# Performance work log

Hardware: AMD Instinct MI355X
Metric: run time of the kernel (lower is better)

## Reference

```python
import jax, jax.numpy as jnp
import numpy as np

HIDDEN = 2048
NH = 32          # num attention heads
NKV = 8          # num key/value heads
HD = HIDDEN // NH  # head_dim = 64
ROPE_BASE = 10000.0
NEG_INF = -1e9


def _rope_interleaved(t, positions):
    # t: [b, s, h, d], interleaved RoPE over full head_dim (flash-attn RotaryEmbedding(interleaved=True))
    d = t.shape[-1]
    inv_freq = 1.0 / (ROPE_BASE ** (jnp.arange(0, d, 2, dtype=jnp.float32) / d))
    ang = positions[:, None].astype(jnp.float32) * inv_freq[None, :]  # [s, d/2]
    cos = jnp.cos(ang)[None, :, None, :]
    sin = jnp.sin(ang)[None, :, None, :]
    t1 = t[..., 0::2]
    t2 = t[..., 1::2]
    out_even = t1 * cos - t2 * sin
    out_odd = t1 * sin + t2 * cos
    return jnp.stack([out_even, out_odd], axis=-1).reshape(t.shape)


def setup_inputs() -> dict:
    key = jax.random.key(0)
    k1, k2, k3 = jax.random.split(key, 3)
    B, S = 2, 2048
    x = jax.random.normal(k1, (B, S, HIDDEN), dtype=jnp.float32)
    mask = jnp.ones((B, S), dtype=jnp.int32)  # padding mask, all valid
    total_head_dim = (NH + 2 * NKV) * HD  # 3072
    scale = 1.0 / np.sqrt(HIDDEN)
    w_qkv = jax.random.normal(k2, (HIDDEN, total_head_dim), dtype=jnp.float32) * scale
    w_o = jax.random.normal(k3, (NH * HD, HIDDEN), dtype=jnp.float32) * scale
    return {"x": x, "mask": mask, "w_qkv": w_qkv, "w_o": w_o}


def reference(x, mask, w_qkv, w_o):
    B, S, _ = x.shape
    kv_size = NKV * HD
    qkv = jnp.einsum('bsh,hd->bsd', x, w_qkv)
    q = qkv[..., :HIDDEN].reshape(B, S, NH, HD)
    kv = qkv[..., HIDDEN:].reshape(B, S, 2, NKV, HD)
    pos = jnp.arange(S)  # seqlen_offset = 0 (input_pos None)
    q = _rope_interleaved(q, pos)
    k = _rope_interleaved(kv[:, :, 0], pos)
    v = kv[:, :, 1]
    # GQA: expand kv heads to NH
    groups = NH // NKV
    k = jnp.repeat(k, groups, axis=2)  # [b, s, NH, HD]
    v = jnp.repeat(v, groups, axis=2)
    scores = jnp.einsum('bqhd,bkhd->bhqk', q, k) / np.sqrt(HD)
    causal = jnp.tril(jnp.ones((S, S), dtype=bool))
    key_valid = mask[:, None, None, :] > 0  # [b,1,1,k]
    scores = jnp.where(causal[None, None] & key_valid, scores, NEG_INF)
    probs = jax.nn.softmax(scores, axis=-1)
    attn = jnp.einsum('bhqk,bkhd->bqhd', probs, v)
    # pad_input writes zeros at padded query positions
    attn = attn * (mask[:, :, None, None] > 0)
    attn = attn.reshape(B, S, NH * HD)
    return jnp.einsum('bsd,dh->bsh', attn, w_o)
```

## Files before the change

### kernel.cpp

```cpp
#include <hip/hip_runtime.h>
#include <hip/hip_bf16.h>
#include <cstdint>
#include <cstddef>

typedef __attribute__((ext_vector_type(8))) short bf16x8;
typedef __attribute__((ext_vector_type(4))) float f32x4;

static constexpr int CB  = 2;
static constexpr int CS  = 2048;
static constexpr int CH  = 2048;
static constexpr int CNH = 32;
static constexpr int CNKV = 8;
static constexpr int CHD = 64;
static constexpr int CTHD = 3072;

__device__ __forceinline__ void gload_lds16(const void* g, void* l) {
  __builtin_amdgcn_global_load_lds(
      (const __attribute__((address_space(1))) unsigned int*)g,
      (__attribute__((address_space(3))) unsigned int*)l, 16, 0, 0);
}

__device__ __forceinline__ unsigned short bfbits(float f) {
  __hip_bfloat16 h = __float2bfloat16(f);
  return *(unsigned short*)&h;
}

__device__ __forceinline__ float b2f(unsigned short s) {
  const unsigned u = (unsigned)s << 16;
  return __uint_as_float(u);
}

__global__ void conv_bf16(const float* __restrict__ in, __hip_bfloat16* __restrict__ out, int n) {
  const int i = (blockIdx.x * 256 + threadIdx.x) * 4;
  if (i >= n) return;
  const float4 v = *(const float4*)(in + i);
  out[i]     = __float2bfloat16(v.x);
  out[i + 1] = __float2bfloat16(v.y);
  out[i + 2] = __float2bfloat16(v.z);
  out[i + 3] = __float2bfloat16(v.w);
}

__global__ void trig_table(float2* __restrict__ tab) {
  const int idx = blockIdx.x * 256 + threadIdx.x;
  const int s = idx >> 5, i = idx & 31;
  const float inv = exp2f(-(float)i * (13.287712379549449f / 32.0f));
  const float ang = (float)s * inv;
  tab[idx] = make_float2(cosf(ang), sinf(ang));
}

__global__ __launch_bounds__(256) void transpose_conv(const float* __restrict__ in,
                                                      __hip_bfloat16* __restrict__ out,
                                                      int R, int Cc) {
  __shared__ float t[32][33];
  const int nbx = Cc >> 5;
  const int bx = blockIdx.x % nbx, by = blockIdx.x / nbx;
  const int c0 = bx << 5, r0 = by << 5;
  const int tx = threadIdx.x & 31, ty = threadIdx.x >> 5;
#pragma unroll
  for (int j = 0; j < 32; j += 8)
    t[ty + j][tx] = in[(size_t)(r0 + ty + j) * Cc + c0 + tx];
  __syncthreads();
#pragma unroll
  for (int j = 0; j < 32; j += 8)
    out[(size_t)(c0 + ty + j) * R + r0 + tx] = __float2bfloat16(t[tx][ty + j]);
}

template <typename OutT>
__global__ __launch_bounds__(512) void gemm_ph(const __hip_bfloat16* __restrict__ A,
                                               const __hip_bfloat16* __restrict__ Bt,
                                               OutT* __restrict__ C, int M, int N, int K) {
  __shared__ __hip_bfloat16 As[2][128 * 64];
  __shared__ __hip_bfloat16 Bs[2][256 * 64];
  const int tid = threadIdx.x;
  const int lane = tid & 63;
  const int wave = tid >> 6;
  const int nTn = N >> 8;
  const int nwg = gridDim.x;
  const int wg = (blockIdx.x & 7) * (nwg >> 3) + (blockIdx.x >> 3);
  const int tm = wg / nTn, tn = wg % nTn;
  const size_t m0 = (size_t)tm * 128, n0 = (size_t)tn * 256;
  const __hip_bfloat16* Ag = A + m0 * K;
  const __hip_bfloat16* Bg = Bt + n0 * K;
  const int wr = wave >> 2, wc = wave & 3;
  const int rsel = lane & 15, hi = lane >> 4;

  f32x4 acc[4][4];
#pragma unroll
  for (int mf = 0; mf < 4; ++mf)
#pragma unroll
    for (int nf = 0; nf < 4; ++nf) acc[mf][nf] = (f32x4){0.f, 0.f, 0.f, 0.f};

  auto stageA = [&](int u) {
    const int k0 = u << 6, buf = u & 1;
#pragma unroll
    for (int i = 0; i < 2; ++i) {
      const int c = i * 512 + tid;
      const int r = c >> 3;
      const int swz = ((c & 7) ^ (r & 7)) << 3;
      gload_lds16(Ag + (size_t)r * K + k0 + swz, &As[buf][(i * 512 + wave * 64) * 8]);
    }
  };
  auto stageB = [&](int u) {
    const int k0 = u << 6, buf = u & 1;
#pragma unroll
    for (int i = 0; i < 4; ++i) {
      const int c = i * 512 + tid;
      const int r = c >> 3;
      const int swz = ((c & 7) ^ (r & 7)) << 3;
      gload_lds16(Bg + (size_t)r * K + k0 + swz, &Bs[buf][(i * 512 + wave * 64) * 8]);
    }
  };

  bf16x8 af[4][2];
  auto readA = [&](int buf) {
#pragma unroll
    for (int mf = 0; mf < 4; ++mf) {
      const int row = wr * 64 + mf * 16 + rsel;
      const int r7 = row & 7;
      af[mf][0] = *(const bf16x8*)&As[buf][row * 64 + ((hi ^ r7) << 3)];
      af[mf][1] = *(const bf16x8*)&As[buf][row * 64 + (((4 | hi) ^ r7) << 3)];
    }
  };
  auto mm = [&](int buf, int nfb) {
    bf16x8 bfr[2][2];
#pragma unroll
    for (int nf = 0; nf < 2; ++nf) {
      const int row = wc * 64 + (nfb + nf) * 16 + rsel;
      const int r7 = row & 7;
      bfr[nf][0] = *(const bf16x8*)&Bs[buf][row * 64 + ((hi ^ r7) << 3)];
      bfr[nf][1] = *(const bf16x8*)&Bs[buf][row * 64 + (((4 | hi) ^ r7) << 3)];
    }
    __builtin_amdgcn_s_setprio(1);
#pragma unroll
    for (int mf = 0; mf < 4; ++mf)
#pragma unroll
      for (int nf = 0; nf < 2; ++nf)
#pragma unroll
        for (int kk = 0; kk < 2; ++kk)
          acc[mf][nfb + nf] =
              __builtin_amdgcn_mfma_f32_16x16x32_bf16(af[mf][kk], bfr[nf][kk], acc[mf][nfb + nf], 0, 0, 0);
    __builtin_amdgcn_s_setprio(0);
  };

  const int T = K >> 7;
  const int UMAX = 2 * T;
  stageA(0); stageB(0); stageA(1); stageB(1);

  for (int t = 0; t < T; ++t) {
    const int u0 = 2 * t, u1 = 2 * t + 1;
    asm volatile("s_waitcnt vmcnt(2)" ::: "memory");
    __builtin_amdgcn_sched_barrier(0);
    __builtin_amdgcn_s_barrier();
    __builtin_amdgcn_sched_barrier(0);
    if (t >= 1) stageB(u1);
    readA(0);
    mm(0, 0);
    __builtin_amdgcn_sched_barrier(0);
    __builtin_amdgcn_s_barrier();
    __builtin_amdgcn_sched_barrier(0);
    if (u0 + 2 < UMAX) stageA(u0 + 2);
    mm(0, 2);
    if (t == T - 1) {
      asm volatile("s_waitcnt vmcnt(0)" ::: "memory");
    } else {
      asm volatile("s_waitcnt vmcnt(2)" ::: "memory");
    }
    __builtin_amdgcn_sched_barrier(0);
    __builtin_amdgcn_s_barrier();
    __builtin_amdgcn_sched_barrier(0);
    if (u0 + 2 < UMAX) stageB(u0 + 2);
    readA(1);
    mm(1, 0);
    __builtin_amdgcn_sched_barrier(0);
    __builtin_amdgcn_s_barrier();
    __builtin_amdgcn_sched_barrier(0);
    if (u1 + 2 < UMAX) stageA(u1 + 2);
    mm(1, 2);
  }

  const int rowb = hi << 2;
#pragma unroll
  for (int mf = 0; mf < 4; ++mf)
#pragma unroll
    for (int nf = 0; nf < 4; ++nf) {
      const size_t r0 = m0 + wr * 64 + mf * 16 + rowb;
      const size_t cc = n0 + wc * 64 + nf * 16 + rsel;
#pragma unroll
      for (int j = 0; j < 4; ++j) {
        const float v = acc[mf][nf][j];
        if constexpr (sizeof(OutT) == 4)
          C[(r0 + j) * N + cc] = v;
        else
          C[(r0 + j) * N + cc] = __float2bfloat16(v);
      }
    }
}

__global__ void rope_extract(const __hip_bfloat16* __restrict__ qkv,
                             const float2* __restrict__ tab,
                             __hip_bfloat16* __restrict__ Q,
                             __hip_bfloat16* __restrict__ Kr) {
  const int idx = blockIdx.x * 256 + threadIdx.x;
  const int t8 = idx & 7;
  const int hs = (idx >> 3) % 40;
  const int r = idx / (40 * 8);
  const int srow = r & (CS - 1);
  const int b = r >> 11;
  const int colbase = (hs < CNH) ? hs * CHD : CH + (hs - CNH) * CHD;
  const bf16x8 v = *(const bf16x8*)(qkv + (size_t)r * CTHD + colbase + t8 * 8);
  const float2* tp = tab + srow * 32 + t8 * 4;
  const float scl = (hs < CNH) ? 0.18033688011112042f : 1.0f;
  union { unsigned short u[8]; bf16x8 v8; } o;
#pragma unroll
  for (int p = 0; p < 4; ++p) {
    const float t1 = b2f((unsigned short)v[2 * p]);
    const float t2 = b2f((unsigned short)v[2 * p + 1]);
    const float2 cs_ = tp[p];
    o.u[2 * p]     = bfbits((t1 * cs_.x - t2 * cs_.y) * scl);
    o.u[2 * p + 1] = bfbits((t1 * cs_.y + t2 * cs_.x) * scl);
  }
  __hip_bfloat16* dst;
  if (hs < CNH)
    dst = Q + ((((size_t)b * CNH + hs) * CS + srow) * CHD + t8 * 8);
  else
    dst = Kr + ((((size_t)b * CNKV + (hs - CNH)) * CS + srow) * CHD + t8 * 8);
  *(bf16x8*)dst = o.v8;
}

__global__ __launch_bounds__(256) void v_transpose(const __hip_bfloat16* __restrict__ qkv,
                                                   __hip_bfloat16* __restrict__ VT) {
  __shared__ __hip_bfloat16 t[64][72];
  const int bi = blockIdx.x;
  const int stile = bi & 31;
  const int kvh = (bi >> 5) & 7;
  const int b = bi >> 8;
  const int tx = threadIdx.x & 63;
  const int ty = threadIdx.x >> 6;
  const int s0 = stile * 64;
#pragma unroll
  for (int j = 0; j < 16; ++j) {
    const int sl = ty * 16 + j;
    t[sl][tx] = qkv[(size_t)(b * CS + s0 + sl) * CTHD + (CH + CNKV * CHD) + kvh * CHD + tx];
  }
  __syncthreads();
#pragma unroll
  for (int j = 0; j < 16; ++j) {
    const int dl = ty * 16 + j;
    VT[(((size_t)b * CNKV + kvh) * CHD + dl) * CS + s0 + tx] = t[tx][dl];
  }
}

__global__ __launch_bounds__(256) void attn_fa(const __hip_bfloat16* __restrict__ Q,
                                               const __hip_bfloat16* __restrict__ Kr,
                                               const __hip_bfloat16* __restrict__ VT,
                                               const int* __restrict__ mask,
                                               __hip_bfloat16* __restrict__ O) {
  __shared__ __hip_bfloat16 Ks[2][64 * 64];
  __shared__ __hip_bfloat16 Vs[64 * 64];
  __shared__ __hip_bfloat16 P4[4][16][72];
  const int kvh = blockIdx.x & 7;
  const int slot = blockIdx.x >> 3;
  const int qw = 127 - (slot >> 1);
  const int b = slot & 1;
  const int tid = threadIdx.x;
  const int wave = tid >> 6, lane = tid & 63;
  const int h = kvh * 4 + wave;
  const int q0 = qw * 16;
  const int rsel = lane & 15;
  const int hi = lane >> 4;
  const int k8 = hi * 8;
  const int rowb = hi * 4;
  const int qr = q0 + rsel;
  const __hip_bfloat16* Qp = Q + (((size_t)b * CNH + h) * CS + q0) * CHD;
  const __hip_bfloat16* Kp = Kr + ((size_t)b * CNKV + kvh) * CS * CHD;
  const __hip_bfloat16* Vp = VT + ((size_t)b * CNKV + kvh) * CHD * CS;
  const int* mp = mask + b * CS;
  __hip_bfloat16(*P)[72] = P4[wave];

  bf16x8 qf[2];
  qf[0] = *(const bf16x8*)(Qp + rsel * CHD + k8);
  qf[1] = *(const bf16x8*)(Qp + rsel * CHD + 32 + k8);

  f32x4 o[4];
#pragma unroll
  for (int nt = 0; nt < 4; ++nt) o[nt] = (f32x4){0.f, 0.f, 0.f, 0.f};
  float mrun = -3e38f, lrun = 0.f;

  const int nkb = (qw >> 2) + 1;

  auto stageK = [&](int buf, int key0) {
#pragma unroll
    for (int half = 0; half < 2; ++half) {
      const int c = half * 256 + tid;
      const int r = c >> 3;
      const int swz = ((c & 7) ^ (r & 7)) * 8;
      gload_lds16(Kp + (size_t)(key0 + r) * CHD + swz,
                  &Ks[buf][(half * 256 + wave * 64) * 8]);
    }
  };
  auto stageV = [&](int key0) {
#pragma unroll
    for (int half = 0; half < 2; ++half) {
      const int c = half * 256 + tid;
      const int r = c >> 3;
      const int swz = ((c & 7) ^ (r & 7)) * 8;
      gload_lds16(Vp + (size_t)r * CS + key0 + swz,
                  &Vs[(half * 256 + wave * 64) * 8]);
    }
  };

  int mcur = mp[lane], mnext = 0;
  stageK(0, 0);
  __syncthreads();

  for (int t = 0; t < nkb; ++t) {
    const int cur = t & 1;
    const int key0 = t * 64;
    const bool last = (t == nkb - 1);
    stageV(key0);
    if (!last) {
      stageK(cur ^ 1, key0 + 64);
      mnext = mp[key0 + 64 + lane];
    }
    const unsigned long long kvbits = __ballot(mcur > 0);
    const int sz = rsel & 7;
    bf16x8 kc[8];
#pragma unroll
    for (int kt = 0; kt < 4; ++kt) {
      const int row = (kt * 16 + rsel) * 64;
      kc[kt * 2]     = *(const bf16x8*)&Ks[cur][row + ((hi ^ sz) << 3)];
      kc[kt * 2 + 1] = *(const bf16x8*)&Ks[cur][row + (((hi ^ 4) ^ sz) << 3)];
    }
    f32x4 st[4];
#pragma unroll
    for (int kt = 0; kt < 4; ++kt) {
      f32x4 s = (f32x4){0.f, 0.f, 0.f, 0.f};
      s = __builtin_amdgcn_mfma_f32_16x16x32_bf16(kc[kt * 2], qf[0], s, 0, 0, 0);
      s = __builtin_amdgcn_mfma_f32_16x16x32_bf16(kc[kt * 2 + 1], qf[1], s, 0, 0, 0);
      st[kt] = s;
    }
    if (!(kvbits == ~0ull && !last)) {
#pragma unroll
      for (int kt = 0; kt < 4; ++kt)
#pragma unroll
        for (int j = 0; j < 4; ++j) {
          const int idx = kt * 16 + rowb + j;
          const bool bad = !((kvbits >> idx) & 1ull) || (last && key0 + idx > qr);
          if (bad) st[kt][j] = -1e9f;
        }
    }
    float pmax = st[0][0];
#pragma unroll
    for (int kt = 0; kt < 4; ++kt)
#pragma unroll
      for (int j = 0; j < 4; ++j) pmax = fmaxf(pmax, st[kt][j]);
    pmax = fmaxf(pmax, __shfl_xor(pmax, 16));
    pmax = fmaxf(pmax, __shfl_xor(pmax, 32));
    if (__any(pmax > mrun + 8.0f)) {
      const float mn = fmaxf(mrun, pmax);
      const float al = exp2f(mrun - mn);
      mrun = mn;
      lrun *= al;
#pragma unroll
      for (int nt = 0; nt < 4; ++nt)
#pragma unroll
        for (int j = 0; j < 4; ++j) o[nt][j] *= al;
    }
    float ps = 0.f;
#pragma unroll
    for (int kt = 0; kt < 4; ++kt)
#pragma unroll
      for (int j = 0; j < 4; ++j) {
        const float p = exp2f(st[kt][j] - mrun);
        st[kt][j] = p;
        ps += p;
      }
    ps += __shfl_xor(ps, 16);
    ps += __shfl_xor(ps, 32);
    lrun += ps;
#pragma unroll
    for (int kt = 0; kt < 4; ++kt) {
      ushort4 pk;
      pk.x = bfbits(st[kt][0]);
      pk.y = bfbits(st[kt][1]);
      pk.z = bfbits(st[kt][2]);
      pk.w = bfbits(st[kt][3]);
      *(ushort4*)&P[rsel][kt * 16 + rowb] = pk;
    }
    __syncthreads();
    const bf16x8 pb0 = *(const bf16x8*)&P[rsel][k8];
    const bf16x8 pb1 = *(const bf16x8*)&P[rsel][32 + k8];
    bf16x8 vf[8];
#pragma unroll
    for (int nt = 0; nt < 4; ++nt) {
      const int row = (nt * 16 + rsel) * 64;
      vf[nt * 2]     = *(const bf16x8*)&Vs[row + ((hi ^ sz) << 3)];
      vf[nt * 2 + 1] = *(const bf16x8*)&Vs[row + (((hi ^ 4) ^ sz) << 3)];
    }
#pragma unroll
    for (int nt = 0; nt < 4; ++nt) {
      o[nt] = __builtin_amdgcn_mfma_f32_16x16x32_bf16(vf[nt * 2], pb0, o[nt], 0, 0, 0);
      o[nt] = __builtin_amdgcn_mfma_f32_16x16x32_bf16(vf[nt * 2 + 1], pb1, o[nt], 0, 0, 0);
    }
    __syncthreads();
    mcur = mnext;
  }

  const float qm = (mp[qr] > 0) ? 1.0f : 0.0f;
  const float inv = qm / fmaxf(lrun, 1e-20f);
  __hip_bfloat16* Orow = O + (((size_t)b * CS + qr) * CNH + h) * CHD;
#pragma unroll
  for (int nt = 0; nt < 4; ++nt) {
    ushort4 ok;
    ok.x = bfbits(o[nt][0] * inv);
    ok.y = bfbits(o[nt][1] * inv);
    ok.z = bfbits(o[nt][2] * inv);
    ok.w = bfbits(o[nt][3] * inv);
    *(ushort4*)(Orow + nt * 16 + rowb) = ok;
  }
}

extern "C" void kernel_launch(void* const* d_in, const int* in_sizes, int n_in,
                              void* d_out, int out_size, void* d_ws, size_t ws_size,
                              hipStream_t stream) {
  const float* x = (const float*)d_in[0];
  const int* mask = (const int*)d_in[1];
  const float* w_qkv = (const float*)d_in[2];
  const float* w_o = (const float*)d_in[3];
  float* out = (float*)d_out;

  char* ws = (char*)d_ws;
  size_t off = 0;
  auto alloc = [&](size_t bytes) {
    char* p = ws + off;
    off += (bytes + 255) & ~(size_t)255;
    return p;
  };
  const size_t M = (size_t)CB * CS;
  __hip_bfloat16* x_bf  = (__hip_bfloat16*)alloc(M * CH * 2);
  __hip_bfloat16* wqkvT = (__hip_bfloat16*)alloc((size_t)CTHD * CH * 2);
  __hip_bfloat16* woT   = (__hip_bfloat16*)alloc((size_t)CH * CH * 2);
  float2*         tab   = (float2*)alloc((size_t)CS * 32 * sizeof(float2));
  __hip_bfloat16* qkv   = (__hip_bfloat16*)alloc(M * CTHD * 2);
  __hip_bfloat16* Qb    = (__hip_bfloat16*)alloc((size_t)CB * CNH * CS * CHD * 2);
  __hip_bfloat16* Kb    = (__hip_bfloat16*)alloc((size_t)CB * CNKV * CS * CHD * 2);
  __hip_bfloat16* VTb   = (__hip_bfloat16*)alloc((size_t)CB * CNKV * CHD * CS * 2);
  __hip_bfloat16* attnb = (__hip_bfloat16*)alloc(M * CH * 2);

  conv_bf16<<<(int)(M * CH / 4 / 256), 256, 0, stream>>>(x, x_bf, (int)(M * CH));
  transpose_conv<<<(CTHD / 32) * (CH / 32), 256, 0, stream>>>(w_qkv, wqkvT, CH, CTHD);
  transpose_conv<<<(CH / 32) * (CH / 32), 256, 0, stream>>>(w_o, woT, CH, CH);
  trig_table<<<(CS * 32) / 256, 256, 0, stream>>>(tab);
  gemm_ph<__hip_bfloat16><<<(int)(M / 128) * (CTHD / 256), 512, 0, stream>>>(
      x_bf, wqkvT, qkv, (int)M, CTHD, CH);
  rope_extract<<<(int)(M * 40 * 8 / 256), 256, 0, stream>>>(qkv, tab, Qb, Kb);
  v_transpose<<<CB * CNKV * 32, 256, 0, stream>>>(qkv, VTb);
  attn_fa<<<CB * CNKV * 128, 256, 0, stream>>>(Qb, Kb, VTb, mask, attnb);
  gemm_ph<float><<<(int)(M / 128) * (CH / 256), 512, 0, stream>>>(
      attnb, woT, out, (int)M, CH, CH);
}
```

Baseline: 231.3 us.

## Merge prepass and rope/V-transpose launches; double-buffer V tiles in attention

Four preprocessing kernels (x conversion, two weight transposes, trig table) become one launch that dispatches on block index, and the RoPE extract and V transpose become a second merged launch. This removes launch gaps and the tail idle time between small kernels. In the attention kernel, V tiles are now double-buffered and prefetched together with the next K tile. V fragments are read before the softmax, and one __syncthreads per iteration is dropped. This uses more LDS per block, which may reduce occupancy, and relies on the per-wave P buffer not needing a block-wide barrier.

New measurement: 223.3 us, median of 2. 1.04x faster.

```diff
diff --git a/kernel.cpp b/kernel.cpp
--- a/kernel.cpp
+++ b/kernel.cpp
@@ -30,30 +30,40 @@
   return __uint_as_float(u);
 }
 
-__global__ void conv_bf16(const float* __restrict__ in, __hip_bfloat16* __restrict__ out, int n) {
-  const int i = (blockIdx.x * 256 + threadIdx.x) * 4;
-  if (i >= n) return;
-  const float4 v = *(const float4*)(in + i);
-  out[i]     = __float2bfloat16(v.x);
-  out[i + 1] = __float2bfloat16(v.y);
-  out[i + 2] = __float2bfloat16(v.z);
-  out[i + 3] = __float2bfloat16(v.w);
-}
-
-__global__ void trig_table(float2* __restrict__ tab) {
-  const int idx = blockIdx.x * 256 + threadIdx.x;
-  const int s = idx >> 5, i = idx & 31;
-  const float inv = exp2f(-(float)i * (13.287712379549449f / 32.0f));
-  const float ang = (float)s * inv;
-  tab[idx] = make_float2(cosf(ang), sinf(ang));
-}
-
-__global__ __launch_bounds__(256) void transpose_conv(const float* __restrict__ in,
-                                                      __hip_bfloat16* __restrict__ out,
-                                                      int R, int Cc) {
+__global__ __launch_bounds__(256) void prepass_fused(const float* __restrict__ x,
+                                                     const float* __restrict__ w_qkv,
+                                                     const float* __restrict__ w_o,
+                                                     __hip_bfloat16* __restrict__ x_bf,
+                                                     __hip_bfloat16* __restrict__ wqkvT,
+                                                     __hip_bfloat16* __restrict__ woT,
+                                                     float2* __restrict__ tab) {
   __shared__ float t[32][33];
+  const int bid = blockIdx.x;
+  if (bid < 8192) {
+    const int i = (bid * 256 + threadIdx.x) * 4;
+    const float4 v = *(const float4*)(x + i);
+    x_bf[i]     = __float2bfloat16(v.x);
+    x_bf[i + 1] = __float2bfloat16(v.y);
+    x_bf[i + 2] = __float2bfloat16(v.z);
+    x_bf[i + 3] = __float2bfloat16(v.w);
+    return;
+  }
+  if (bid >= 18432) {
+    const int idx = (bid - 18432) * 256 + threadIdx.x;
+    const int s = idx >> 5, i = idx & 31;
+    const float inv = exp2f(-(float)i * (13.287712379549449f / 32.0f));
+    const float ang = (float)s * inv;
+    tab[idx] = make_float2(cosf(ang), sinf(ang));
+    return;
+  }
+  const float* in;
+  __hip_bfloat16* out;
+  int R, Cc, lb;
+  if (bid < 14336) { in = w_qkv; out = wqkvT; R = CH; Cc = CTHD; lb = 8192; }
+  else             { in = w_o;   out = woT;   R = CH; Cc = CH;   lb = 14336; }
+  const int lbid = bid - lb;
   const int nbx = Cc >> 5;
-  const int bx = blockIdx.x % nbx, by = blockIdx.x / nbx;
+  const int bx = lbid % nbx, by = lbid / nbx;
   const int c0 = bx << 5, r0 = by << 5;
   const int tx = threadIdx.x & 31, ty = threadIdx.x >> 5;
 #pragma unroll
@@ -196,41 +206,42 @@
     }
 }
 
-__global__ void rope_extract(const __hip_bfloat16* __restrict__ qkv,
-                             const float2* __restrict__ tab,
-                             __hip_bfloat16* __restrict__ Q,
-                             __hip_bfloat16* __restrict__ Kr) {
-  const int idx = blockIdx.x * 256 + threadIdx.x;
-  const int t8 = idx & 7;
-  const int hs = (idx >> 3) % 40;
-  const int r = idx / (40 * 8);
-  const int srow = r & (CS - 1);
-  const int b = r >> 11;
-  const int colbase = (hs < CNH) ? hs * CHD : CH + (hs - CNH) * CHD;
-  const bf16x8 v = *(const bf16x8*)(qkv + (size_t)r * CTHD + colbase + t8 * 8);
-  const float2* tp = tab + srow * 32 + t8 * 4;
-  const float scl = (hs < CNH) ? 0.18033688011112042f : 1.0f;
-  union { unsigned short u[8]; bf16x8 v8; } o;
-#pragma unroll
-  for (int p = 0; p < 4; ++p) {
-    const float t1 = b2f((unsigned short)v[2 * p]);
-    const float t2 = b2f((unsigned short)v[2 * p + 1]);
-    const float2 cs_ = tp[p];
-    o.u[2 * p]     = bfbits((t1 * cs_.x - t2 * cs_.y) * scl);
-    o.u[2 * p + 1] = bfbits((t1 * cs_.y + t2 * cs_.x) * scl);
-  }
-  __hip_bfloat16* dst;
-  if (hs < CNH)
-    dst = Q + ((((size_t)b * CNH + hs) * CS + srow) * CHD + t8 * 8);
-  else
-    dst = Kr + ((((size_t)b * CNKV + (hs - CNH)) * CS + srow) * CHD + t8 * 8);
-  *(bf16x8*)dst = o.v8;
-}
-
-__global__ __launch_bounds__(256) void v_transpose(const __hip_bfloat16* __restrict__ qkv,
-                                                   __hip_bfloat16* __restrict__ VT) {
+__global__ __launch_bounds__(256) void ropevt_fused(const __hip_bfloat16* __restrict__ qkv,
+                                                    const float2* __restrict__ tab,
+                                                    __hip_bfloat16* __restrict__ Q,
+                                                    __hip_bfloat16* __restrict__ Kr,
+                                                    __hip_bfloat16* __restrict__ VT) {
   __shared__ __hip_bfloat16 t[64][72];
-  const int bi = blockIdx.x;
+  const int bid = blockIdx.x;
+  if (bid < 5120) {
+    const int idx = bid * 256 + threadIdx.x;
+    const int t8 = idx & 7;
+    const int hs = (idx >> 3) % 40;
+    const int r = idx / (40 * 8);
+    const int srow = r & (CS - 1);
+    const int b = r >> 11;
+    const int colbase = (hs < CNH) ? hs * CHD : CH + (hs - CNH) * CHD;
+    const bf16x8 v = *(const bf16x8*)(qkv + (size_t)r * CTHD + colbase + t8 * 8);
+    const float2* tp = tab + srow * 32 + t8 * 4;
+    const float scl = (hs < CNH) ? 0.18033688011112042f : 1.0f;
+    union { unsigned short u[8]; bf16x8 v8; } o;
+#pragma unroll
+    for (int p = 0; p < 4; ++p) {
+      const float t1 = b2f((unsigned short)v[2 * p]);
+      const float t2 = b2f((unsigned short)v[2 * p + 1]);
+      const float2 cs_ = tp[p];
+      o.u[2 * p]     = bfbits((t1 * cs_.x - t2 * cs_.y) * scl);
+      o.u[2 * p + 1] = bfbits((t1 * cs_.y + t2 * cs_.x) * scl);
+    }
+    __hip_bfloat16* dst;
+    if (hs < CNH)
+      dst = Q + ((((size_t)b * CNH + hs) * CS + srow) * CHD + t8 * 8);
+    else
+      dst = Kr + ((((size_t)b * CNKV + (hs - CNH)) * CS + srow) * CHD + t8 * 8);
+    *(bf16x8*)dst = o.v8;
+    return;
+  }
+  const int bi = bid - 5120;
   const int stile = bi & 31;
   const int kvh = (bi >> 5) & 7;
   const int b = bi >> 8;
@@ -256,7 +267,7 @@
                                                const int* __restrict__ mask,
                                                __hip_bfloat16* __restrict__ O) {
   __shared__ __hip_bfloat16 Ks[2][64 * 64];
-  __shared__ __hip_bfloat16 Vs[64 * 64];
+  __shared__ __hip_bfloat16 Vs[2][64 * 64];
   __shared__ __hip_bfloat16 P4[4][16][72];
   const int kvh = blockIdx.x & 7;
   const int slot = blockIdx.x >> 3;
@@ -288,38 +299,29 @@
 
   const int nkb = (qw >> 2) + 1;
 
-  auto stageK = [&](int buf, int key0) {
+  auto stage = [&](int buf, int key0) {
 #pragma unroll
     for (int half = 0; half < 2; ++half) {
       const int c = half * 256 + tid;
       const int r = c >> 3;
       const int swz = ((c & 7) ^ (r & 7)) * 8;
-      gload_lds16(Kp + (size_t)(key0 + r) * CHD + swz,
-                  &Ks[buf][(half * 256 + wave * 64) * 8]);
-    }
-  };
-  auto stageV = [&](int key0) {
-#pragma unroll
-    for (int half = 0; half < 2; ++half) {
-      const int c = half * 256 + tid;
-      const int r = c >> 3;
-      const int swz = ((c & 7) ^ (r & 7)) * 8;
-      gload_lds16(Vp + (size_t)r * CS + key0 + swz,
-                  &Vs[(half * 256 + wave * 64) * 8]);
+      __hip_bfloat16* kd = &Ks[buf][(half * 256 + wave * 64) * 8];
+      __hip_bfloat16* vd = &Vs[buf][(half * 256 + wave * 64) * 8];
+      gload_lds16(Kp + (size_t)(key0 + r) * CHD + swz, kd);
+      gload_lds16(Vp + (size_t)r * CS + key0 + swz, vd);
     }
   };
 
   int mcur = mp[lane], mnext = 0;
-  stageK(0, 0);
+  stage(0, 0);
   __syncthreads();
 
   for (int t = 0; t < nkb; ++t) {
     const int cur = t & 1;
     const int key0 = t * 64;
     const bool last = (t == nkb - 1);
-    stageV(key0);
     if (!last) {
-      stageK(cur ^ 1, key0 + 64);
+      stage(cur ^ 1, key0 + 64);
       mnext = mp[key0 + 64 + lane];
     }
     const unsigned long long kvbits = __ballot(mcur > 0);
@@ -338,6 +340,13 @@
       s = __builtin_amdgcn_mfma_f32_16x16x32_bf16(kc[kt * 2], qf[0], s, 0, 0, 0);
       s = __builtin_amdgcn_mfma_f32_16x16x32_bf16(kc[kt * 2 + 1], qf[1], s, 0, 0, 0);
       st[kt] = s;
+    }
+    bf16x8 vf[8];
+#pragma unroll
+    for (int nt = 0; nt < 4; ++nt) {
+      const int row = (nt * 16 + rsel) * 64;
+      vf[nt * 2]     = *(const bf16x8*)&Vs[cur][row + ((hi ^ sz) << 3)];
+      vf[nt * 2 + 1] = *(const bf16x8*)&Vs[cur][row + (((hi ^ 4) ^ sz) << 3)];
     }
     if (!(kvbits == ~0ull && !last)) {
 #pragma unroll
@@ -387,16 +396,8 @@
       pk.w = bfbits(st[kt][3]);
       *(ushort4*)&P[rsel][kt * 16 + rowb] = pk;
     }
-    __syncthreads();
     const bf16x8 pb0 = *(const bf16x8*)&P[rsel][k8];
     const bf16x8 pb1 = *(const bf16x8*)&P[rsel][32 + k8];
-    bf16x8 vf[8];
-#pragma unroll
-    for (int nt = 0; nt < 4; ++nt) {
-      const int row = (nt * 16 + rsel) * 64;
-      vf[nt * 2]     = *(const bf16x8*)&Vs[row + ((hi ^ sz) << 3)];
-      vf[nt * 2 + 1] = *(const bf16x8*)&Vs[row + (((hi ^ 4) ^ sz) << 3)];
-    }
 #pragma unroll
     for (int nt = 0; nt < 4; ++nt) {
       o[nt] = __builtin_amdgcn_mfma_f32_16x16x32_bf16(vf[nt * 2], pb0, o[nt], 0, 0, 0);
@@ -447,14 +448,10 @@
   __hip_bfloat16* VTb   = (__hip_bfloat16*)alloc((size_t)CB * CNKV * CHD * CS * 2);
   __hip_bfloat16* attnb = (__hip_bfloat16*)alloc(M * CH * 2);
 
-  conv_bf16<<<(int)(M * CH / 4 / 256), 256, 0, stream>>>(x, x_bf, (int)(M * CH));
-  transpose_conv<<<(CTHD / 32) * (CH / 32), 256, 0, stream>>>(w_qkv, wqkvT, CH, CTHD);
-  transpose_conv<<<(CH / 32) * (CH / 32), 256, 0, stream>>>(w_o, woT, CH, CH);
-  trig_table<<<(CS * 32) / 256, 256, 0, stream>>>(tab);
+  prepass_fused<<<18688, 256, 0, stream>>>(x, w_qkv, w_o, x_bf, wqkvT, woT, tab);
   gemm_ph<__hip_bfloat16><<<(int)(M / 128) * (CTHD / 256), 512, 0, stream>>>(
       x_bf, wqkvT, qkv, (int)M, CTHD, CH);
-  rope_extract<<<(int)(M * 40 * 8 / 256), 256, 0, stream>>>(qkv, tab, Qb, Kb);
-  v_transpose<<<CB * CNKV * 32, 256, 0, stream>>>(qkv, VTb);
+  ropevt_fused<<<5632, 256, 0, stream>>>(qkv, tab, Qb, Kb, VTb);
   attn_fa<<<CB * CNKV * 128, 256, 0, stream>>>(Qb, Kb, VTb, mask, attnb);
   gemm_ph<float><<<(int)(M / 128) * (CH / 256), 512, 0, stream>>>(
       attnb, woT, out, (int)M, CH, CH);
```
